# Kernel tuning notes

Measured on AMD Instinct MI355X. Metric: run time of the kernel, lower is better.

Reference implementation:

```python
import jax, jax.numpy as jnp
import numpy as np

DIM = 256
HEADS = 8
HEAD_DIM = DIM // HEADS
WS = 7            # window size
SHIFT = 3         # shift size
H = 56
W = 56
B = 32
WA = WS * WS      # window area = 49
NWH, NWW = H // WS, W // WS
NW = NWH * NWW    # windows per image


def _make_attn_mask():
    # replicate the torch mask construction for the shifted windows
    img = np.zeros((H, W), dtype=np.float32)
    cnt = 0
    for hs in (slice(0, -WS), slice(-WS, -SHIFT), slice(-SHIFT, None)):
        for ws_ in (slice(0, -WS), slice(-WS, -SHIFT), slice(-SHIFT, None)):
            img[hs, ws_] = cnt
            cnt += 1
    mw = img.reshape(NWH, WS, NWW, WS).transpose(0, 2, 1, 3).reshape(-1, WA)  # (nW, 49)
    diff = mw[:, None, :] - mw[:, :, None]                                    # (nW, 49, 49)
    return np.where(diff != 0, -100.0, 0.0).astype(np.float32)


def _make_rel_index():
    coords = np.stack(np.meshgrid(np.arange(WS), np.arange(WS), indexing='ij')).reshape(2, -1)
    rel = coords[:, :, None] - coords[:, None, :]        # (2, 49, 49)
    rel = rel.transpose(1, 2, 0) + (WS - 1)              # shift to >= 0
    rel[..., 0] *= 2 * WS - 1
    return rel.sum(-1).astype(np.int32)                  # (49, 49) in [0, 169)


def setup_inputs() -> dict:
    key = jax.random.key(0)
    ks = jax.random.split(key, 12)
    s = 0.02
    inp = {
        'x': jax.random.normal(ks[0], (B, H, W, DIM), dtype=jnp.float32),
        'ln1_w': jnp.ones((DIM,), jnp.float32), 'ln1_b': jnp.zeros((DIM,), jnp.float32),
        'qkv_w': s * jax.random.normal(ks[1], (3 * DIM, DIM), jnp.float32),
        'qkv_b': jnp.zeros((3 * DIM,), jnp.float32),
        'rpb_table': s * jax.random.normal(ks[2], ((2 * WS - 1) ** 2, HEADS), jnp.float32),
        'proj_w': s * jax.random.normal(ks[3], (DIM, DIM), jnp.float32),
        'proj_b': jnp.zeros((DIM,), jnp.float32),
        'ln2_w': jnp.ones((DIM,), jnp.float32), 'ln2_b': jnp.zeros((DIM,), jnp.float32),
        'fc1_w': s * jax.random.normal(ks[4], (4 * DIM, DIM), jnp.float32),
        'fc1_b': jnp.zeros((4 * DIM,), jnp.float32),
        'ln3_w': jnp.ones((4 * DIM,), jnp.float32), 'ln3_b': jnp.zeros((4 * DIM,), jnp.float32),
        'fc2_w': s * jax.random.normal(ks[5], (DIM, 4 * DIM), jnp.float32),
        'fc2_b': jnp.zeros((DIM,), jnp.float32),
        'attn_mask': jnp.asarray(_make_attn_mask()),     # (nW, 49, 49)
        'rel_index': jnp.asarray(_make_rel_index()),     # (49, 49) int32
    }
    return inp


def _ln(x, w, b, eps=1e-5):
    m = jnp.mean(x, axis=-1, keepdims=True)
    v = jnp.mean((x - m) ** 2, axis=-1, keepdims=True)
    return (x - m) * jax.lax.rsqrt(v + eps) * w + b


def reference(x, ln1_w, ln1_b, qkv_w, qkv_b, rpb_table, proj_w, proj_b,
              ln2_w, ln2_b, fc1_w, fc1_b, ln3_w, ln3_b, fc2_w, fc2_b,
              attn_mask, rel_index):
    Bn, Hn, Wn, C = x.shape
    # ---- attention branch ----
    y = _ln(x, ln1_w, ln1_b)
    sh = jnp.roll(y, (-SHIFT, -SHIFT), axis=(1, 2))
    # window partition: (B, H, W, C) -> (B*nW, 49, C)
    win = sh.reshape(Bn, NWH, WS, NWW, WS, C).transpose(0, 1, 3, 2, 4, 5).reshape(Bn * NW, WA, C)
    qkv = win @ qkv_w.T + qkv_b                              # (Bw, 49, 3C)
    qkv = qkv.reshape(Bn * NW, WA, 3, HEADS, HEAD_DIM).transpose(2, 0, 3, 1, 4)
    q, k, v = qkv[0], qkv[1], qkv[2]                         # (Bw, h, 49, d)
    scale = HEAD_DIM ** -0.5
    attn = jnp.einsum('bhqd,bhkd->bhqk', q * scale, k)       # (Bw, h, 49, 49)
    bias = rpb_table[rel_index]                              # (49, 49, h)
    attn = attn + jnp.transpose(bias, (2, 0, 1))[None]
    attn = attn.reshape(Bn, NW, HEADS, WA, WA) + attn_mask[None, :, None]
    attn = jax.nn.softmax(attn, axis=-1).reshape(Bn * NW, HEADS, WA, WA)
    out = jnp.einsum('bhqk,bhkd->bhqd', attn, v)             # (Bw, h, 49, d)
    out = out.transpose(0, 2, 1, 3).reshape(Bn * NW, WA, C)
    out = out @ proj_w.T + proj_b
    # window reverse + un-shift
    out = out.reshape(Bn, NWH, NWW, WS, WS, C).transpose(0, 1, 3, 2, 4, 5).reshape(Bn, Hn, Wn, C)
    out = jnp.roll(out, (SHIFT, SHIFT), axis=(1, 2))
    x = x + out
    # ---- MLP branch (note: extra LayerNorm inside MLP per source) ----
    z = _ln(x, ln2_w, ln2_b)
    h = jax.nn.gelu(z @ fc1_w.T + fc1_b, approximate=False)
    h = _ln(h, ln3_w, ln3_b)
    x = x + (h @ fc2_w.T + fc2_b)
    return x
```

## Files before the change

kernel.cpp:

```cpp
#include <hip/hip_runtime.h>
#include <hip/hip_bf16.h>
#include <math.h>

typedef __attribute__((ext_vector_type(8))) short bf16x8;
typedef __attribute__((ext_vector_type(4))) float f32x4;
typedef __attribute__((ext_vector_type(4))) float f4;
typedef __attribute__((ext_vector_type(8))) unsigned short us8;
typedef __attribute__((ext_vector_type(4))) unsigned short us4;
typedef unsigned short u16;
typedef unsigned int u32;

#define HEADS 8
#define SHIFT_ 3
#define HIMG 56
#define WIMG 56
#define WA 49
#define NTOK 100352
#define NPAIR 16384

static __device__ __forceinline__ float bf2f(u16 v){ return __uint_as_float(((u32)v)<<16); }
static __device__ __forceinline__ u16 f2bf(float f){
  u32 u = __float_as_uint(f);
  return (u16)((u + 0x7fffu + ((u>>16)&1u)) >> 16);
}
static __device__ __forceinline__ float wsum(float v){
  #pragma unroll
  for (int off=32; off>0; off>>=1) v += __shfl_xor(v, off, 64);
  return v;
}
static __device__ __forceinline__ void glds16(const u16* g, u16* l){
  __builtin_amdgcn_global_load_lds(
      (const __attribute__((address_space(1))) unsigned int*)g,
      (__attribute__((address_space(3))) unsigned int*)l, 16, 0, 0);
}
static __device__ __forceinline__ int tok2pix(int row){
  int bw = row / 49, t = row - bw*49;
  int b  = bw >> 6,  w = bw & 63;
  int wh = w >> 3,   ww = w & 7;
  int th = t / 7,    tw = t - th*7;
  int r = wh*7 + th + SHIFT_; if (r >= HIMG) r -= HIMG;
  int c = ww*7 + tw + SHIFT_; if (c >= WIMG) c -= WIMG;
  return (b*HIMG + r)*WIMG + c;
}
static __device__ __forceinline__ float gelu_f(float x){
  float x2 = x*x;
  float u  = x*(0.7978845608028654f + 0.0356774081363001f*x2);
  float e  = __expf(u+u);
  float th = 1.0f - 2.0f*__builtin_amdgcn_rcpf(1.0f+e);
  return 0.5f*x*(1.0f+th);
}

__global__ void zero_kernel(float* __restrict__ p){
  p[blockIdx.x*256 + threadIdx.x] = 0.f;
}

template<int C, int ISBF>
__global__ void ln_stats_kernel(const void* __restrict__ srcv, float* __restrict__ stats){
  int wave = threadIdx.x >> 6, lane = threadIdx.x & 63;
  int tok = blockIdx.x*4 + wave;
  float s=0.f, s2=0.f;
  if (ISBF == 0){
    const float* p = (const float*)srcv + (size_t)tok*C;
    #pragma unroll
    for (int i=0;i<C/256;i++){
      f4 v = *(const f4*)(p + lane*4*(C/256) + i*4);
      #pragma unroll
      for (int e=0;e<4;e++){ float f=v[e]; s+=f; s2+=f*f; }
    }
  } else {
    const u16* p = (const u16*)srcv + (size_t)tok*C;
    #pragma unroll
    for (int i=0;i<C/512;i++){
      us8 v = *(const us8*)(p + lane*8*(C/512) + i*8);
      #pragma unroll
      for (int e=0;e<8;e++){ float f=bf2f(v[e]); s+=f; s2+=f*f; }
    }
  }
  s = wsum(s); s2 = wsum(s2);
  if (lane==0){
    float mean = s/(float)C;
    float var  = s2/(float)C - mean*mean;
    stats[2*tok]   = mean;
    stats[2*tok+1] = rsqrtf(var + 1e-5f);
  }
}

__global__ void ln_apply_kernel(const float* __restrict__ src, u16* __restrict__ dst){
  int wave = threadIdx.x >> 6, lane = threadIdx.x & 63;
  int tok = blockIdx.x*4 + wave;
  const float* p = src + (size_t)tok*256;
  f4 a = *(const f4*)(p + lane*4);
  float s = a[0]+a[1]+a[2]+a[3];
  float s2 = a[0]*a[0]+a[1]*a[1]+a[2]*a[2]+a[3]*a[3];
  s = wsum(s); s2 = wsum(s2);
  float mean = s*(1.f/256.f);
  float var  = s2*(1.f/256.f) - mean*mean;
  float rstd = rsqrtf(var + 1e-5f);
  us4 o;
  #pragma unroll
  for (int e=0;e<4;e++) o[e] = f2bf((a[e]-mean)*rstd);
  *(us4*)(dst + (size_t)tok*256 + lane*4) = o;
}

__global__ void prep_weights(
    const float* __restrict__ qkv_w, const float* __restrict__ qkv_b,
    const float* __restrict__ ln1w,  const float* __restrict__ ln1b,
    const float* __restrict__ fc1_w, const float* __restrict__ fc1_b,
    const float* __restrict__ ln2w,  const float* __restrict__ ln2b,
    const float* __restrict__ fc2_w, const float* __restrict__ fc2_b,
    const float* __restrict__ ln3w,  const float* __restrict__ ln3b,
    const float* __restrict__ proj_w, const float* __restrict__ proj_b,
    u16* __restrict__ wq, float* __restrict__ bq,
    u16* __restrict__ w1, float* __restrict__ b1,
    u16* __restrict__ w2, float* __restrict__ b2,
    u16* __restrict__ wp, float* __restrict__ bp,
    float* __restrict__ cs2)
{
  int wave = threadIdx.x>>6, lane = threadIdx.x&63;
  int n = blockIdx.x*4 + wave;
  const float *W,*lw,*lb,*bs; u16* WO; float* BO; int K, row, noln, docs;
  if (n < 768)      { W=qkv_w; lw=ln1w; lb=ln1b; bs=qkv_b; WO=wq; BO=bq; K=256;  row=n;      noln=0; docs=0; }
  else if (n < 1792){ W=fc1_w; lw=ln2w; lb=ln2b; bs=fc1_b; WO=w1; BO=b1; K=256;  row=n-768;  noln=0; docs=0; }
  else if (n < 2048){ W=fc2_w; lw=ln3w; lb=ln3b; bs=fc2_b; WO=w2; BO=b2; K=1024; row=n-1792; noln=0; docs=1; }
  else              { W=proj_w; lw=nullptr; lb=nullptr; bs=proj_b; WO=wp; BO=bp; K=256; row=n-2048; noln=1; docs=0; }
  float dot = 0.f, cs = 0.f;
  for (int k=lane; k<K; k+=64){
    float wv = W[(size_t)row*K + k];
    if (noln){
      WO[(size_t)row*K + k] = f2bf(wv);
    } else {
      dot += wv * lb[k];
      u16 q = f2bf(wv * lw[k]);
      WO[(size_t)row*K + k] = q;
      cs += bf2f(q);
    }
  }
  dot = wsum(dot);
  if (docs){ cs = wsum(cs); if (lane==0) cs2[row] = cs; }
  if (lane==0) BO[row] = bs[row] + dot;
}

template<int SMODE, int EPI, int SWAP>
__global__ __launch_bounds__(256)
void gemm9(const void* __restrict__ Av, const u16* __restrict__ Bt,
           const float* __restrict__ stats, float* __restrict__ hstats,
           const float* __restrict__ biasf, const float* __restrict__ resid,
           const float* __restrict__ colsum, void* __restrict__ outv,
           int K, int NT, int CHUNK)
{
  constexpr int BM=128, BN=128, BK=32;
  __shared__ u16 smem[16384];
  int b = blockIdx.x;
  int linear = (b & 7)*CHUNK + (b >> 3);
  int mt = linear / NT, nt = linear - mt*NT;
  int m0 = mt*BM, n0 = nt*BN;
  int tid  = threadIdx.x;
  int lane = tid & 63, wave = tid >> 6;
  int wr = wave >> 1, wc = wave & 1;
  int lc16 = lane & 15, g = lane >> 4;
  int nsteps = K >> 5;

  const u16* asrc[2];
  const u16* bsrc[2];
  #pragma unroll
  for (int i=0;i<2;i++){
    int c = tid + i*256;
    int row = c >> 2, ch = (c & 3) ^ (row & 3);
    if (SMODE <= 1){
      int grow = (SMODE==0) ? tok2pix(m0+row) : (m0+row);
      asrc[i] = (const u16*)Av + (size_t)grow*K + ch*8;
    }
    bsrc[i] = Bt + (size_t)(n0+row)*K + ch*8;
  }
  float smean[2], srstd[2];
  if (SMODE == 3){
    #pragma unroll
    for (int i=0;i<2;i++){
      int grow = m0 + ((tid + i*256) >> 2);
      smean[i] = stats[2*grow]; srstd[i] = stats[2*grow+1];
    }
  }

  f32x4 acc[4][4];
  #pragma unroll
  for (int i=0;i<4;i++)
    #pragma unroll
    for (int j=0;j<4;j++){ acc[i][j][0]=0.f; acc[i][j][1]=0.f; acc[i][j][2]=0.f; acc[i][j][3]=0.f; }

  if (SMODE <= 1){
    #pragma unroll
    for (int i=0;i<2;i++) glds16(asrc[i], smem + i*2048 + wave*512);
    #pragma unroll
    for (int i=0;i<2;i++) glds16(bsrc[i], smem + 8192 + i*2048 + wave*512);
    __syncthreads();
    for (int t=0; t<nsteps; ++t){
      int cur = t & 1, nxt = cur ^ 1;
      if (t+1 < nsteps){
        int kt1 = (t+1) << 5;
        #pragma unroll
        for (int i=0;i<2;i++) glds16(asrc[i]+kt1, smem + nxt*4096 + i*2048 + wave*512);
        #pragma unroll
        for (int i=0;i<2;i++) glds16(bsrc[i]+kt1, smem + 8192 + nxt*4096 + i*2048 + wave*512);
      }
      const u16* Ap = smem + cur*4096;
      const u16* Bp = smem + 8192 + cur*4096;
      bf16x8 af[4], bfr[4];
      #pragma unroll
      for (int mi=0;mi<4;mi++){
        int r = wr*64 + mi*16 + lc16;
        u32 byte = (u32)(r*64 + g*16) ^ ((u32)(r&3)<<4);
        af[mi] = *(const bf16x8*)(Ap + (byte>>1));
      }
      #pragma unroll
      for (int ni=0;ni<4;ni++){
        int r = wc*64 + ni*16 + lc16;
        u32 byte = (u32)(r*64 + g*16) ^ ((u32)(r&3)<<4);
        bfr[ni] = *(const bf16x8*)(Bp + (byte>>1));
      }
      #pragma unroll
      for (int mi=0;mi<4;mi++)
        #pragma unroll
        for (int ni=0;ni<4;ni++)
          acc[mi][ni] = SWAP ? __builtin_amdgcn_mfma_f32_16x16x32_bf16(bfr[ni], af[mi], acc[mi][ni], 0, 0, 0)
                             : __builtin_amdgcn_mfma_f32_16x16x32_bf16(af[mi], bfr[ni], acc[mi][ni], 0, 0, 0);
      __syncthreads();
    }
  } else {
    f4 rcurf[2][2];
    #pragma unroll
    for (int i=0;i<2;i++){
      int c = tid + i*256; int row = c>>2, ch = c&3;
      const float* ap = (const float*)Av + (size_t)(m0+row)*K + ch*8;
      rcurf[i][0] = *(const f4*)ap; rcurf[i][1] = *(const f4*)(ap+4);
    }
    for (int t=0; t<nsteps; ++t){
      int kt = t << 5;
      #pragma unroll
      for (int i=0;i<2;i++){
        int c = tid + i*256; int row = c>>2, k8 = (c&3)*8;
        us8 o;
        #pragma unroll
        for (int e=0;e<8;e++){
          float fv = rcurf[i][e>>2][e&3];
          o[e] = f2bf((fv - smean[i])*srstd[i]);
        }
        u32 byte = (u32)(row*64 + k8*2) ^ ((u32)(row&3)<<4);
        *(us8*)(smem + (byte>>1)) = o;
      }
      #pragma unroll
      for (int i=0;i<2;i++) glds16(bsrc[i]+kt, smem + 8192 + i*2048 + wave*512);
      __syncthreads();
      if (t+1 < nsteps){
        int kt1 = kt + 32;
        #pragma unroll
        for (int i=0;i<2;i++){
          int c = tid + i*256; int row = c>>2, ch = c&3;
          const float* ap = (const float*)Av + (size_t)(m0+row)*K + kt1 + ch*8;
          rcurf[i][0] = *(const f4*)ap; rcurf[i][1] = *(const f4*)(ap+4);
        }
      }
      bf16x8 af[4], bfr[4];
      #pragma unroll
      for (int mi=0;mi<4;mi++){
        int r = wr*64 + mi*16 + lc16;
        u32 byte = (u32)(r*64 + g*16) ^ ((u32)(r&3)<<4);
        af[mi] = *(const bf16x8*)(smem + (byte>>1));
      }
      #pragma unroll
      for (int ni=0;ni<4;ni++){
        int r = wc*64 + ni*16 + lc16;
        u32 byte = (u32)(r*64 + g*16) ^ ((u32)(r&3)<<4);
        bfr[ni] = *(const bf16x8*)(smem + 8192 + (byte>>1));
      }
      #pragma unroll
      for (int mi=0;mi<4;mi++)
        #pragma unroll
        for (int ni=0;ni<4;ni++)
          acc[mi][ni] = SWAP ? __builtin_amdgcn_mfma_f32_16x16x32_bf16(bfr[ni], af[mi], acc[mi][ni], 0, 0, 0)
                             : __builtin_amdgcn_mfma_f32_16x16x32_bf16(af[mi], bfr[ni], acc[mi][ni], 0, 0, 0);
      __syncthreads();
    }
  }

  int lr = lane >> 4;
  if (EPI==0){
    u16* Cs = smem;
    #pragma unroll
    for (int mi=0;mi<4;mi++){
      #pragma unroll
      for (int ni=0;ni<4;ni++){
        int cl = wc*64 + ni*16 + lc16;
        float bv = biasf[n0 + cl];
        #pragma unroll
        for (int j=0;j<4;j++){
          int rl = wr*64 + mi*16 + lr*4 + j;
          float v = acc[mi][ni][j] + bv;
          u32 byte = (u32)(rl*256 + cl*2) ^ ((u32)(rl&7)<<4);
          Cs[byte>>1] = f2bf(v);
        }
      }
    }
    __syncthreads();
    #pragma unroll
    for (int i=0;i<8;i++){
      int c = tid + i*256;
      int rl = c>>4, c0 = (c&15)*8;
      u32 byte = (u32)(rl*256 + c0*2) ^ ((u32)(rl&7)<<4);
      us8 v = *(const us8*)(Cs + (byte>>1));
      int row = m0 + rl, col = n0 + c0;
      int which = col>>8, hh = (col>>5)&7, d0 = col&31;
      int bwi = row/49, t = row - bwi*49;
      *(us8*)((u16*)outv + ((size_t)which*NPAIR + bwi*8 + hh)*(WA*32) + t*32 + d0) = v;
    }
  } else if (EPI==2){
    u16* Cs = smem;
    #pragma unroll
    for (int mi=0;mi<4;mi++){
      int rl = wr*64 + mi*16 + lc16;
      float ss = 0.f, sq = 0.f;
      #pragma unroll
      for (int ni=0;ni<4;ni++){
        int cl = wc*64 + ni*16 + g*4;
        f4 bv = *(const f4*)(biasf + n0 + cl);
        us4 o;
        #pragma unroll
        for (int j=0;j<4;j++){
          float v = gelu_f(acc[mi][ni][j] + bv[j]);
          ss += v; sq += v*v;
          o[j] = f2bf(v);
        }
        u32 byte = (u32)(rl*256 + cl*2) ^ ((u32)(rl&7)<<4);
        *(us4*)(Cs + (byte>>1)) = o;
      }
      ss += __shfl_xor(ss, 16, 64); ss += __shfl_xor(ss, 32, 64);
      sq += __shfl_xor(sq, 16, 64); sq += __shfl_xor(sq, 32, 64);
      if (g==0){
        int grow = m0 + rl;
        atomicAdd(&hstats[2*grow],   ss);
        atomicAdd(&hstats[2*grow+1], sq);
      }
    }
    __syncthreads();
    #pragma unroll
    for (int i=0;i<8;i++){
      int c = tid + i*256;
      int rl = c>>4, c0 = (c&15)*8;
      u32 byte = (u32)(rl*256 + c0*2) ^ ((u32)(rl&7)<<4);
      us8 v = *(const us8*)(Cs + (byte>>1));
      int row = m0 + rl, col = n0 + c0;
      *(us8*)((u16*)outv + (size_t)row*1024 + col) = v;
    }
  } else {
    float* Cs = (float*)smem;
    #pragma unroll
    for (int hp=0; hp<2; hp++){
      if (hp) __syncthreads();
      if (wc == hp){
        #pragma unroll
        for (int mi=0;mi<4;mi++){
          float rs4[4], mr4[4];
          if (EPI==4){
            #pragma unroll
            for (int j=0;j<4;j++){
              int grow = m0 + wr*64 + mi*16 + lr*4 + j;
              float s = stats[2*grow], q = stats[2*grow+1];
              float mean = s*(1.f/1024.f);
              float var  = q*(1.f/1024.f) - mean*mean;
              rs4[j] = rsqrtf(var + 1e-5f);
              mr4[j] = mean*rs4[j];
            }
          }
          #pragma unroll
          for (int ni=0;ni<4;ni++){
            int cl = ni*16 + lc16;
            int col = n0 + hp*64 + cl;
            float bv = biasf[col];
            float cw = (EPI==4) ? colsum[col] : 0.f;
            #pragma unroll
            for (int j=0;j<4;j++){
              int rl = wr*64 + mi*16 + lr*4 + j;
              float v;
              if (EPI==4) v = acc[mi][ni][j]*rs4[j] - mr4[j]*cw + bv;
              else        v = acc[mi][ni][j] + bv;
              u32 byte = (u32)(rl*256 + cl*4) ^ ((u32)(rl&7)<<4);
              *(float*)((char*)Cs + byte) = v;
            }
          }
        }
      }
      __syncthreads();
      #pragma unroll
      for (int i=0;i<8;i++){
        int c = tid + i*256;
        int row = c>>4, ch = c&15;
        u32 byte = (u32)(row*256 + ch*16) ^ ((u32)(row&7)<<4);
        f4 v = *(const f4*)((const char*)Cs + byte);
        int grow = m0 + row, col = n0 + hp*64 + ch*4;
        size_t addr;
        if (EPI==1) addr = (size_t)tok2pix(grow)*256 + col;
        else        addr = (size_t)grow*256 + col;
        f4 rr = *(const f4*)(resid + addr);
        v += rr;
        *(f4*)((float*)outv + addr) = v;
      }
    }
  }
}

__global__ void attn_mfma_kernel(
    const u16* __restrict__ qkv,
    const float* __restrict__ rpb,
    const int* __restrict__ rel,
    const float* __restrict__ mask,
    u16* __restrict__ outb)
{
  __shared__ u16 Kls[4][64*32];
  __shared__ u16 Vt [4][32*64];
  __shared__ u16 Pls[4][64*64];
  int wave = threadIdx.x>>6, lane = threadIdx.x&63;
  int pair = blockIdx.x*4 + wave;
  int bw = pair>>3, h = pair&7, w = bw&63;
  int lc = lane&15, g = lane>>4;
  const u16* qg = qkv + (size_t)pair*(WA*32);
  const u16* kg = qg + (size_t)NPAIR*(WA*32);
  const u16* vg = qg + (size_t)2*NPAIR*(WA*32);
  u16* Kp = &Kls[wave][0];
  u16* Vp = &Vt[wave][0];
  u16* Pp = &Pls[wave][0];

  #pragma unroll
  for (int i=0;i<4;i++){
    int idx = i*64 + lane;
    int r = idx>>2, seg = idx&3;
    us8 kv, vv;
    if (r < WA){
      kv = *(const us8*)(kg + r*32 + seg*8);
      vv = *(const us8*)(vg + r*32 + seg*8);
    } else {
      #pragma unroll
      for (int e=0;e<8;e++){ kv[e]=0; vv[e]=0; }
    }
    *(us8*)(Kp + r*32 + seg*8) = kv;
    #pragma unroll
    for (int e=0;e<8;e++){
      int d = seg*8 + e;
      u32 byte = ((u32)(d*128 + r*2)) ^ ((u32)(d&7)<<4);
      Vp[byte>>1] = vv[e];
    }
  }

  bf16x8 qa[4];
  #pragma unroll
  for (int mi=0;mi<4;mi++){
    int r = mi*16 + lc;
    if (r < WA) qa[mi] = *(const bf16x8*)(qg + r*32 + g*8);
    else { bf16x8 z;
           #pragma unroll
           for (int e=0;e<8;e++) z[e]=0; qa[mi]=z; }
  }

  f32x4 acc[4][4];
  #pragma unroll
  for (int i=0;i<4;i++)
    #pragma unroll
    for (int j=0;j<4;j++){ acc[i][j][0]=0.f; acc[i][j][1]=0.f; acc[i][j][2]=0.f; acc[i][j][3]=0.f; }
  __syncthreads();
  #pragma unroll
  for (int ni=0;ni<4;ni++){
    bf16x8 kb = *(const bf16x8*)(Kp + (ni*16+lc)*32 + g*8);
    #pragma unroll
    for (int mi=0;mi<4;mi++)
      acc[mi][ni] = __builtin_amdgcn_mfma_f32_16x16x32_bf16(qa[mi], kb, acc[mi][ni], 0, 0, 0);
  }

  const float scale = 0.17677669529663689f;
  float rinv[4][4];
  #pragma unroll
  for (int mi=0;mi<4;mi++){
    #pragma unroll
    for (int jr=0;jr<4;jr++){
      int i = mi*16 + g*4 + jr;
      float sv[4];
      #pragma unroll
      for (int ni=0;ni<4;ni++){
        int j = ni*16 + lc;
        float s;
        if (i < WA && j < WA){
          s = acc[mi][ni][jr]*scale + rpb[rel[i*WA+j]*8 + h] + mask[((size_t)w*WA + i)*WA + j];
        } else s = -1e9f;
        sv[ni] = s;
      }
      float mx = fmaxf(fmaxf(sv[0],sv[1]), fmaxf(sv[2],sv[3]));
      #pragma unroll
      for (int off=1; off<16; off<<=1) mx = fmaxf(mx, __shfl_xor(mx, off, 64));
      float sum = 0.f;
      #pragma unroll
      for (int ni=0;ni<4;ni++){ sv[ni] = __expf(sv[ni]-mx); sum += sv[ni]; }
      #pragma unroll
      for (int off=1; off<16; off<<=1) sum += __shfl_xor(sum, off, 64);
      rinv[mi][jr] = __builtin_amdgcn_rcpf(sum);
      #pragma unroll
      for (int ni=0;ni<4;ni++){
        int j = ni*16 + lc;
        u32 byte = ((u32)(i*128 + j*2)) ^ ((u32)(i&7)<<4);
        Pp[byte>>1] = f2bf(sv[ni]);
      }
    }
  }

  bf16x8 vb[2][2];
  #pragma unroll
  for (int kk=0;kk<2;kk++)
    #pragma unroll
    for (int ni=0;ni<2;ni++){
      int d = ni*16 + lc;
      u32 byte = ((u32)(d*128 + kk*64 + g*16)) ^ ((u32)(d&7)<<4);
      vb[kk][ni] = *(const bf16x8*)(Vp + (byte>>1));
    }
  f32x4 aco[4][2];
  #pragma unroll
  for (int i=0;i<4;i++)
    #pragma unroll
    for (int j=0;j<2;j++){ aco[i][j][0]=0.f; aco[i][j][1]=0.f; aco[i][j][2]=0.f; aco[i][j][3]=0.f; }
  #pragma unroll
  for (int mi=0;mi<4;mi++){
    int r = mi*16 + lc;
    #pragma unroll
    for (int kk=0;kk<2;kk++){
      u32 byte = ((u32)(r*128 + kk*64 + g*16)) ^ ((u32)(r&7)<<4);
      bf16x8 pa = *(const bf16x8*)(Pp + (byte>>1));
      #pragma unroll
      for (int ni=0;ni<2;ni++)
        aco[mi][ni] = __builtin_amdgcn_mfma_f32_16x16x32_bf16(pa, vb[kk][ni], aco[mi][ni], 0, 0, 0);
    }
  }

  u16* Op = Kp;
  #pragma unroll
  for (int mi=0;mi<4;mi++){
    #pragma unroll
    for (int jr=0;jr<4;jr++){
      int i = mi*16 + g*4 + jr;
      if (i < WA){
        float rv = rinv[mi][jr];
        #pragma unroll
        for (int ni=0;ni<2;ni++)
          Op[i*32 + ni*16 + lc] = f2bf(aco[mi][ni][jr]*rv);
      }
    }
  }
  __syncthreads();
  size_t obase = (size_t)(bw*WA)*256 + h*32;
  #pragma unroll
  for (int i=0;i<4;i++){
    int c = i*64 + lane;
    if (c < WA*4){
      int t = c>>2, seg = c&3;
      *(us8*)(outb + obase + (size_t)t*256 + seg*8) = *(const us8*)(Op + t*32 + seg*8);
    }
  }
}

extern "C" void kernel_launch(void* const* d_in, const int* in_sizes, int n_in,
                              void* d_out, int out_size, void* d_ws, size_t ws_size,
                              hipStream_t stream) {
  const float* x      = (const float*)d_in[0];
  const float* ln1w   = (const float*)d_in[1];
  const float* ln1b   = (const float*)d_in[2];
  const float* qkv_w  = (const float*)d_in[3];
  const float* qkv_b  = (const float*)d_in[4];
  const float* rpb    = (const float*)d_in[5];
  const float* proj_w = (const float*)d_in[6];
  const float* proj_b = (const float*)d_in[7];
  const float* ln2w   = (const float*)d_in[8];
  const float* ln2b   = (const float*)d_in[9];
  const float* fc1_w  = (const float*)d_in[10];
  const float* fc1_b  = (const float*)d_in[11];
  const float* ln3w   = (const float*)d_in[12];
  const float* ln3b   = (const float*)d_in[13];
  const float* fc2_w  = (const float*)d_in[14];
  const float* fc2_b  = (const float*)d_in[15];
  const float* amask  = (const float*)d_in[16];
  const int*   rel    = (const int*)d_in[17];
  float* out = (float*)d_out;

  char* ws = (char*)d_ws;
  float* hstats = (float*)(ws);
  float* statsB = (float*)(ws +  802816);
  float* bq     = (float*)(ws + 1605632);
  float* b1     = (float*)(ws + 1608704);
  float* b2     = (float*)(ws + 1612800);
  float* bp     = (float*)(ws + 1613824);
  float* cs2    = (float*)(ws + 1614848);
  u16*   wq     = (u16*)  (ws + 1615872);
  u16*   w1     = (u16*)  (ws + 2009088);
  u16*   w2     = (u16*)  (ws + 2533376);
  u16*   wp     = (u16*)  (ws + 3057664);
  const size_t P0 = 3188736;
  u16*   qkvbuf = (u16*)(ws + P0);
  u16*   attno  = (u16*)(ws + P0 + 154140672);
  u16*   xb     = (u16*)(ws + P0 + 154140672);
  u16*   hbuf   = (u16*)(ws + P0);
  u16*   x1b    = (u16*)(ws + P0 + 205520896);
  const int bigws = (ws_size >= (size_t)(P0 + 205520896ull + 51380224ull));

  prep_weights<<<576,256,0,stream>>>(qkv_w,qkv_b,ln1w,ln1b, fc1_w,fc1_b,ln2w,ln2b,
                                     fc2_w,fc2_b,ln3w,ln3b, proj_w,proj_b,
                                     wq,bq, w1,b1, w2,b2, wp,bp, cs2);
  ln_apply_kernel<<<NTOK/4,256,0,stream>>>(x, xb);
  gemm9<0,0,0><<<784*6,256,0,stream>>>(xb, wq, nullptr, nullptr, bq, nullptr, nullptr, qkvbuf, 256, 6, 588);
  attn_mfma_kernel<<<NPAIR/4,256,0,stream>>>(qkvbuf, rpb, rel, amask, attno);
  gemm9<1,1,0><<<784*2,256,0,stream>>>(attno, wp, nullptr, nullptr, bp, x, nullptr, out, 256, 2, 196);
  zero_kernel<<<784,256,0,stream>>>(hstats);
  if (bigws){
    ln_apply_kernel<<<NTOK/4,256,0,stream>>>(out, x1b);
    gemm9<1,2,1><<<784*8,256,0,stream>>>(x1b, w1, nullptr, hstats, b1, nullptr, nullptr, hbuf, 256, 8, 784);
  } else {
    ln_stats_kernel<256,0><<<NTOK/4,256,0,stream>>>(out, statsB);
    gemm9<3,2,1><<<784*8,256,0,stream>>>(out, w1, statsB, hstats, b1, nullptr, nullptr, hbuf, 256, 8, 784);
  }
  gemm9<1,4,0><<<784*2,256,0,stream>>>(hbuf, w2, hstats, nullptr, b2, out, cs2, out, 1024, 2, 196);
}
```

Baseline: 587.5 us.

## Fuse LN2 stats and bf16 copy into proj epilogue; change LDS swizzle

The proj GEMM epilogue now also writes a bf16 copy of the residual output and accumulates per-token sum and sum-of-squares into a stats buffer with atomics. The fc1 GEMM then applies LayerNorm algebraically in its epilogue, using the folded weight column sums, so the separate ln_apply pass over the residual stream is dropped. Separately, the LDS layout changes from an XOR swizzle to a rotation-based swizzle on both the load and read sides to alter bank-conflict behavior. The cost is extra atomics in the proj epilogue, a mean/variance computed from raw moments that may lose precision, and a larger workspace requirement.

Measured after the change: 632.8 us. 1.08x slower.

```diff
diff --git a/kernel.cpp b/kernel.cpp
--- a/kernel.cpp
+++ b/kernel.cpp
@@ -114,15 +114,15 @@
     u16* __restrict__ w1, float* __restrict__ b1,
     u16* __restrict__ w2, float* __restrict__ b2,
     u16* __restrict__ wp, float* __restrict__ bp,
-    float* __restrict__ cs2)
+    float* __restrict__ cs1, float* __restrict__ cs2)
 {
   int wave = threadIdx.x>>6, lane = threadIdx.x&63;
   int n = blockIdx.x*4 + wave;
-  const float *W,*lw,*lb,*bs; u16* WO; float* BO; int K, row, noln, docs;
-  if (n < 768)      { W=qkv_w; lw=ln1w; lb=ln1b; bs=qkv_b; WO=wq; BO=bq; K=256;  row=n;      noln=0; docs=0; }
-  else if (n < 1792){ W=fc1_w; lw=ln2w; lb=ln2b; bs=fc1_b; WO=w1; BO=b1; K=256;  row=n-768;  noln=0; docs=0; }
-  else if (n < 2048){ W=fc2_w; lw=ln3w; lb=ln3b; bs=fc2_b; WO=w2; BO=b2; K=1024; row=n-1792; noln=0; docs=1; }
-  else              { W=proj_w; lw=nullptr; lb=nullptr; bs=proj_b; WO=wp; BO=bp; K=256; row=n-2048; noln=1; docs=0; }
+  const float *W,*lw,*lb,*bs; u16* WO; float* BO; float* CS; int K, row, noln;
+  if (n < 768)      { W=qkv_w; lw=ln1w; lb=ln1b; bs=qkv_b; WO=wq; BO=bq; K=256;  row=n;      noln=0; CS=nullptr; }
+  else if (n < 1792){ W=fc1_w; lw=ln2w; lb=ln2b; bs=fc1_b; WO=w1; BO=b1; K=256;  row=n-768;  noln=0; CS=cs1; }
+  else if (n < 2048){ W=fc2_w; lw=ln3w; lb=ln3b; bs=fc2_b; WO=w2; BO=b2; K=1024; row=n-1792; noln=0; CS=cs2; }
+  else              { W=proj_w; lw=nullptr; lb=nullptr; bs=proj_b; WO=wp; BO=bp; K=256; row=n-2048; noln=1; CS=nullptr; }
   float dot = 0.f, cs = 0.f;
   for (int k=lane; k<K; k+=64){
     float wv = W[(size_t)row*K + k];
@@ -136,17 +136,18 @@
     }
   }
   dot = wsum(dot);
-  if (docs){ cs = wsum(cs); if (lane==0) cs2[row] = cs; }
+  if (CS){ cs = wsum(cs); if (lane==0) CS[row] = cs; }
   if (lane==0) BO[row] = bs[row] + dot;
 }
 
 template<int SMODE, int EPI, int SWAP>
 __global__ __launch_bounds__(256)
-void gemm9(const void* __restrict__ Av, const u16* __restrict__ Bt,
-           const float* __restrict__ stats, float* __restrict__ hstats,
-           const float* __restrict__ biasf, const float* __restrict__ resid,
-           const float* __restrict__ colsum, void* __restrict__ outv,
-           int K, int NT, int CHUNK)
+void gemm10(const void* __restrict__ Av, const u16* __restrict__ Bt,
+            const float* __restrict__ stats, float* __restrict__ hstats,
+            const float* __restrict__ biasf, const float* __restrict__ resid,
+            const float* __restrict__ colsum, void* __restrict__ outv,
+            u16* __restrict__ out2, float* __restrict__ stats2,
+            int K, int NT, int CHUNK)
 {
   constexpr int BM=128, BN=128, BK=32;
   __shared__ u16 smem[16384];
@@ -165,12 +166,12 @@
   #pragma unroll
   for (int i=0;i<2;i++){
     int c = tid + i*256;
-    int row = c >> 2, ch = (c & 3) ^ (row & 3);
+    int row = c >> 2, gch = ((c & 3) - (row >> 1)) & 3;
     if (SMODE <= 1){
       int grow = (SMODE==0) ? tok2pix(m0+row) : (m0+row);
-      asrc[i] = (const u16*)Av + (size_t)grow*K + ch*8;
-    }
-    bsrc[i] = Bt + (size_t)(n0+row)*K + ch*8;
+      asrc[i] = (const u16*)Av + (size_t)grow*K + gch*8;
+    }
+    bsrc[i] = Bt + (size_t)(n0+row)*K + gch*8;
   }
   float smean[2], srstd[2];
   if (SMODE == 3){
@@ -208,13 +209,13 @@
       #pragma unroll
       for (int mi=0;mi<4;mi++){
         int r = wr*64 + mi*16 + lc16;
-        u32 byte = (u32)(r*64 + g*16) ^ ((u32)(r&3)<<4);
+        u32 byte = (u32)(r*64) + ((u32)((g + (r>>1)) & 3) << 4);
         af[mi] = *(const bf16x8*)(Ap + (byte>>1));
       }
       #pragma unroll
       for (int ni=0;ni<4;ni++){
         int r = wc*64 + ni*16 + lc16;
-        u32 byte = (u32)(r*64 + g*16) ^ ((u32)(r&3)<<4);
+        u32 byte = (u32)(r*64) + ((u32)((g + (r>>1)) & 3) << 4);
         bfr[ni] = *(const bf16x8*)(Bp + (byte>>1));
       }
       #pragma unroll
@@ -229,22 +230,22 @@
     f4 rcurf[2][2];
     #pragma unroll
     for (int i=0;i<2;i++){
-      int c = tid + i*256; int row = c>>2, ch = c&3;
-      const float* ap = (const float*)Av + (size_t)(m0+row)*K + ch*8;
+      int c = tid + i*256; int row = c>>2, gch = ((c&3) - (row>>1)) & 3;
+      const float* ap = (const float*)Av + (size_t)(m0+row)*K + gch*8;
       rcurf[i][0] = *(const f4*)ap; rcurf[i][1] = *(const f4*)(ap+4);
     }
     for (int t=0; t<nsteps; ++t){
       int kt = t << 5;
       #pragma unroll
       for (int i=0;i<2;i++){
-        int c = tid + i*256; int row = c>>2, k8 = (c&3)*8;
+        int c = tid + i*256; int row = c>>2, s = c&3;
         us8 o;
         #pragma unroll
         for (int e=0;e<8;e++){
           float fv = rcurf[i][e>>2][e&3];
           o[e] = f2bf((fv - smean[i])*srstd[i]);
         }
-        u32 byte = (u32)(row*64 + k8*2) ^ ((u32)(row&3)<<4);
+        u32 byte = (u32)(row*64) + ((u32)s << 4);
         *(us8*)(smem + (byte>>1)) = o;
       }
       #pragma unroll
@@ -254,8 +255,8 @@
         int kt1 = kt + 32;
         #pragma unroll
         for (int i=0;i<2;i++){
-          int c = tid + i*256; int row = c>>2, ch = c&3;
-          const float* ap = (const float*)Av + (size_t)(m0+row)*K + kt1 + ch*8;
+          int c = tid + i*256; int row = c>>2, gch = ((c&3) - (row>>1)) & 3;
+          const float* ap = (const float*)Av + (size_t)(m0+row)*K + kt1 + gch*8;
           rcurf[i][0] = *(const f4*)ap; rcurf[i][1] = *(const f4*)(ap+4);
         }
       }
@@ -263,13 +264,13 @@
       #pragma unroll
       for (int mi=0;mi<4;mi++){
         int r = wr*64 + mi*16 + lc16;
-        u32 byte = (u32)(r*64 + g*16) ^ ((u32)(r&3)<<4);
+        u32 byte = (u32)(r*64) + ((u32)((g + (r>>1)) & 3) << 4);
         af[mi] = *(const bf16x8*)(smem + (byte>>1));
       }
       #pragma unroll
       for (int ni=0;ni<4;ni++){
         int r = wc*64 + ni*16 + lc16;
-        u32 byte = (u32)(r*64 + g*16) ^ ((u32)(r&3)<<4);
+        u32 byte = (u32)(r*64) + ((u32)((g + (r>>1)) & 3) << 4);
         bfr[ni] = *(const bf16x8*)(smem + 8192 + (byte>>1));
       }
       #pragma unroll
@@ -312,20 +313,33 @@
       int bwi = row/49, t = row - bwi*49;
       *(us8*)((u16*)outv + ((size_t)which*NPAIR + bwi*8 + hh)*(WA*32) + t*32 + d0) = v;
     }
-  } else if (EPI==2){
+  } else if (EPI==2 || EPI==5){
     u16* Cs = smem;
     #pragma unroll
     for (int mi=0;mi<4;mi++){
       int rl = wr*64 + mi*16 + lc16;
+      float rs = 1.f, mr = 0.f;
+      if (EPI==5){
+        int grow = m0 + rl;
+        float s = stats[2*grow], q = stats[2*grow+1];
+        float mean = s*(1.f/256.f);
+        float var  = q*(1.f/256.f) - mean*mean;
+        rs = rsqrtf(var + 1e-5f);
+        mr = mean*rs;
+      }
       float ss = 0.f, sq = 0.f;
       #pragma unroll
       for (int ni=0;ni<4;ni++){
         int cl = wc*64 + ni*16 + g*4;
         f4 bv = *(const f4*)(biasf + n0 + cl);
+        f4 cw;
+        if (EPI==5) cw = *(const f4*)(colsum + n0 + cl);
         us4 o;
         #pragma unroll
         for (int j=0;j<4;j++){
-          float v = gelu_f(acc[mi][ni][j] + bv[j]);
+          float v = (EPI==5) ? (acc[mi][ni][j]*rs - mr*cw[j] + bv[j])
+                             : (acc[mi][ni][j] + bv[j]);
+          v = gelu_f(v);
           ss += v; sq += v*v;
           o[j] = f2bf(v);
         }
@@ -402,6 +416,23 @@
         f4 rr = *(const f4*)(resid + addr);
         v += rr;
         *(f4*)((float*)outv + addr) = v;
+        if (EPI==1 && out2){
+          us4 ob;
+          #pragma unroll
+          for (int e=0;e<4;e++) ob[e] = f2bf(v[e]);
+          *(us4*)(out2 + addr) = ob;
+          float ps = v[0]+v[1]+v[2]+v[3];
+          float pq = v[0]*v[0]+v[1]*v[1]+v[2]*v[2]+v[3]*v[3];
+          ps += __shfl_xor(ps, 1, 64); pq += __shfl_xor(pq, 1, 64);
+          ps += __shfl_xor(ps, 2, 64); pq += __shfl_xor(pq, 2, 64);
+          ps += __shfl_xor(ps, 4, 64); pq += __shfl_xor(pq, 4, 64);
+          ps += __shfl_xor(ps, 8, 64); pq += __shfl_xor(pq, 8, 64);
+          if ((tid & 15) == 0){
+            int pix = tok2pix(grow);
+            atomicAdd(&stats2[2*pix],   ps);
+            atomicAdd(&stats2[2*pix+1], pq);
+          }
+        }
       }
     }
   }
@@ -585,39 +616,50 @@
   float* out = (float*)d_out;
 
   char* ws = (char*)d_ws;
-  float* hstats = (float*)(ws);
-  float* statsB = (float*)(ws +  802816);
-  float* bq     = (float*)(ws + 1605632);
-  float* b1     = (float*)(ws + 1608704);
-  float* b2     = (float*)(ws + 1612800);
-  float* bp     = (float*)(ws + 1613824);
-  float* cs2    = (float*)(ws + 1614848);
-  u16*   wq     = (u16*)  (ws + 1615872);
-  u16*   w1     = (u16*)  (ws + 2009088);
-  u16*   w2     = (u16*)  (ws + 2533376);
-  u16*   wp     = (u16*)  (ws + 3057664);
-  const size_t P0 = 3188736;
+  float* stats2 = (float*)(ws);
+  float* hstats = (float*)(ws +  802816);
+  float* statsB = (float*)(ws + 1605632);
+  float* bq     = (float*)(ws + 2408448);
+  float* b1     = (float*)(ws + 2411520);
+  float* b2     = (float*)(ws + 2415616);
+  float* bp     = (float*)(ws + 2416640);
+  float* cs1    = (float*)(ws + 2417664);
+  float* cs2    = (float*)(ws + 2421760);
+  u16*   wq     = (u16*)  (ws + 2422784);
+  u16*   w1     = (u16*)  (ws + 2816000);
+  u16*   w2     = (u16*)  (ws + 3340288);
+  u16*   wp     = (u16*)  (ws + 3864576);
+  const size_t P0 = 3995648;
   u16*   qkvbuf = (u16*)(ws + P0);
   u16*   attno  = (u16*)(ws + P0 + 154140672);
   u16*   xb     = (u16*)(ws + P0 + 154140672);
-  u16*   hbuf   = (u16*)(ws + P0);
-  u16*   x1b    = (u16*)(ws + P0 + 205520896);
-  const int bigws = (ws_size >= (size_t)(P0 + 205520896ull + 51380224ull));
+  u16*   xb2    = (u16*)(ws + P0);
+  u16*   hbuf   = (u16*)(ws + P0 + 51380224);
+  u16*   hbufF  = (u16*)(ws + P0);
+  const int bigws = (ws_size >= (size_t)(P0 + 51380224ull + 205520896ull));
 
   prep_weights<<<576,256,0,stream>>>(qkv_w,qkv_b,ln1w,ln1b, fc1_w,fc1_b,ln2w,ln2b,
                                      fc2_w,fc2_b,ln3w,ln3b, proj_w,proj_b,
-                                     wq,bq, w1,b1, w2,b2, wp,bp, cs2);
+                                     wq,bq, w1,b1, w2,b2, wp,bp, cs1,cs2);
+  zero_kernel<<<1568,256,0,stream>>>(stats2);
   ln_apply_kernel<<<NTOK/4,256,0,stream>>>(x, xb);
-  gemm9<0,0,0><<<784*6,256,0,stream>>>(xb, wq, nullptr, nullptr, bq, nullptr, nullptr, qkvbuf, 256, 6, 588);
+  gemm10<0,0,0><<<784*6,256,0,stream>>>(xb, wq, nullptr, nullptr, bq, nullptr, nullptr, qkvbuf,
+                                        nullptr, nullptr, 256, 6, 588);
   attn_mfma_kernel<<<NPAIR/4,256,0,stream>>>(qkvbuf, rpb, rel, amask, attno);
-  gemm9<1,1,0><<<784*2,256,0,stream>>>(attno, wp, nullptr, nullptr, bp, x, nullptr, out, 256, 2, 196);
-  zero_kernel<<<784,256,0,stream>>>(hstats);
   if (bigws){
-    ln_apply_kernel<<<NTOK/4,256,0,stream>>>(out, x1b);
-    gemm9<1,2,1><<<784*8,256,0,stream>>>(x1b, w1, nullptr, hstats, b1, nullptr, nullptr, hbuf, 256, 8, 784);
+    gemm10<1,1,0><<<784*2,256,0,stream>>>(attno, wp, nullptr, nullptr, bp, x, nullptr, out,
+                                          xb2, stats2, 256, 2, 196);
+    gemm10<1,5,1><<<784*8,256,0,stream>>>(xb2, w1, stats2, hstats, b1, nullptr, cs1, hbuf,
+                                          nullptr, nullptr, 256, 8, 784);
+    gemm10<1,4,0><<<784*2,256,0,stream>>>(hbuf, w2, hstats, nullptr, b2, out, cs2, out,
+                                          nullptr, nullptr, 1024, 2, 196);
   } else {
+    gemm10<1,1,0><<<784*2,256,0,stream>>>(attno, wp, nullptr, nullptr, bp, x, nullptr, out,
+                                          nullptr, nullptr, 256, 2, 196);
     ln_stats_kernel<256,0><<<NTOK/4,256,0,stream>>>(out, statsB);
-    gemm9<3,2,1><<<784*8,256,0,stream>>>(out, w1, statsB, hstats, b1, nullptr, nullptr, hbuf, 256, 8, 784);
-  }
-  gemm9<1,4,0><<<784*2,256,0,stream>>>(hbuf, w2, hstats, nullptr, b2, out, cs2, out, 1024, 2, 196);
-}
+    gemm10<3,2,1><<<784*8,256,0,stream>>>(out, w1, statsB, hstats, b1, nullptr, nullptr, hbufF,
+                                          nullptr, nullptr, 256, 8, 784);
+    gemm10<1,4,0><<<784*2,256,0,stream>>>(hbufF, w2, hstats, nullptr, b2, out, cs2, out,
+                                          nullptr, nullptr, 1024, 2, 196);
+  }
+}
```
